# Optimization experiments

Measured on AMD Instinct MI355X. Metric: run time of the kernel, lower is better.

The kernel has to match this reference:

```python
import jax, jax.numpy as jnp
import numpy as np

B, T, IN, H, OUT = 128, 512, 64, 512, 1
H2 = H // 2


def setup_inputs() -> dict:
    key = jax.random.key(0)
    ks = jax.random.split(key, 16)
    s_in = 1.0 / np.sqrt(H)  # torch LSTM/Linear init scale ~ U(-1/sqrt(H), 1/sqrt(H))
    def u(k, shape, s):
        return jax.random.uniform(k, shape, jnp.float32, -s, s)
    return {
        "x": jax.random.normal(ks[0], (B, T, IN), jnp.float32),
        "W_ih0": u(ks[1], (4 * H, IN), s_in),
        "W_hh0": u(ks[2], (4 * H, H), s_in),
        "b_ih0": u(ks[3], (4 * H,), s_in),
        "b_hh0": u(ks[4], (4 * H,), s_in),
        "W_ih1": u(ks[5], (4 * H, H), s_in),
        "W_hh1": u(ks[6], (4 * H, H), s_in),
        "b_ih1": u(ks[7], (4 * H,), s_in),
        "b_hh1": u(ks[8], (4 * H,), s_in),
        "fc1_w": u(ks[9], (H2, H), s_in),
        "fc1_b": u(ks[10], (H2,), s_in),
        "fc2_w": u(ks[11], (OUT, H2), 1.0 / np.sqrt(H2)),
        "fc2_b": u(ks[12], (OUT,), 1.0 / np.sqrt(H2)),
    }


def _lstm_layer(x, W_ih, W_hh, b_ih, b_hh):
    # x: [B, T, D_in] -> outputs h for all timesteps [B, T, H]
    b, t, _ = x.shape
    h_dim = W_hh.shape[1]
    # precompute input contribution to gates for all timesteps: [T, B, 4H]
    xg = (jnp.einsum('btd,gd->btg', x, W_ih) + b_ih + b_hh).transpose(1, 0, 2)

    def step(carry, xt):
        h, c = carry
        gates = xt + h @ W_hh.T  # [B, 4H]
        i, f, g, o = jnp.split(gates, 4, axis=-1)  # torch gate order i,f,g,o
        i = jax.nn.sigmoid(i)
        f = jax.nn.sigmoid(f)
        g = jnp.tanh(g)
        o = jax.nn.sigmoid(o)
        c = f * c + i * g
        h = o * jnp.tanh(c)
        return (h, c), h

    h0 = jnp.zeros((b, h_dim), x.dtype)
    (_, _), hs = jax.lax.scan(step, (h0, h0), xg)
    return hs.transpose(1, 0, 2)  # [B, T, H]


def reference(x, W_ih0, W_hh0, b_ih0, b_hh0, W_ih1, W_hh1, b_ih1, b_hh1,
              fc1_w, fc1_b, fc2_w, fc2_b):
    h1 = _lstm_layer(x, W_ih0, W_hh0, b_ih0, b_hh0)
    h2 = _lstm_layer(h1, W_ih1, W_hh1, b_ih1, b_hh1)
    last = h2[:, -1, :]  # [B, H]
    z = jax.nn.relu(last @ fc1_w.T + fc1_b)
    return z @ fc2_w.T + fc2_b  # [B, OUT]
```

## Files before the change

kernel.cpp:

```cpp
#include <hip/hip_runtime.h>
#include <hip/hip_fp16.h>

#define BB   128
#define TT   512
#define INS  64
#define HH   512
#define K0   576
#define K1   1024
#define PAD0 584
#define PAD1 1032
#define H2   256
#define FS   16
#define RING 4

typedef _Float16 f16;
typedef f16 f16x4 __attribute__((ext_vector_type(4)));
typedef f16 f16x8 __attribute__((ext_vector_type(8)));
typedef float f32x4 __attribute__((ext_vector_type(4)));

__device__ __forceinline__ float sigmoidf_(float x) {
  return 1.0f / (1.0f + __expf(-x));
}
__device__ __forceinline__ float tanhf_(float x) {
  return 1.0f - 2.0f / (__expf(2.0f * x) + 1.0f);
}

__device__ __forceinline__ f16x8 ldg_h(const f16* p) {
  union { unsigned long long q[2]; f16x8 v; } u;
  const unsigned long long* qp = (const unsigned long long*)p;
  u.q[0] = __hip_atomic_load(qp,     __ATOMIC_RELAXED, __HIP_MEMORY_SCOPE_AGENT);
  u.q[1] = __hip_atomic_load(qp + 1, __ATOMIC_RELAXED, __HIP_MEMORY_SCOPE_AGENT);
  return u.v;
}
__device__ __forceinline__ void stg_h(f16* p, unsigned int pk) {
  __hip_atomic_store((unsigned int*)p, pk, __ATOMIC_RELAXED, __HIP_MEMORY_SCOPE_AGENT);
}
__device__ __forceinline__ int ldf(const int* p) {
  return __hip_atomic_load(p, __ATOMIC_RELAXED, __HIP_MEMORY_SCOPE_AGENT);
}

__global__ __launch_bounds__(256, 1) void lstm_persist(
    const float* __restrict__ x,
    const float* __restrict__ Wih0, const float* __restrict__ Whh0,
    const float* __restrict__ bih0, const float* __restrict__ bhh0,
    const float* __restrict__ Wih1, const float* __restrict__ Whh1,
    const float* __restrict__ bih1, const float* __restrict__ bhh1,
    int* __restrict__ flags, f16* __restrict__ h1ring, f16* __restrict__ h2ring)
{
  extern __shared__ f16 Ws[];

  const int tid  = threadIdx.x;
  const int wg   = blockIdx.x;
  const bool isL1 = (wg >= 128);
  const int w2   = wg & 127;
  const int mg   = w2 >> 6;
  const int ng   = w2 & 63;
  const int wid  = tid >> 6;
  const int lane = tid & 63;

  if (!isL1) {
    for (int e4 = tid; e4 < 32 * (K0 / 4); e4 += 256) {
      int r = e4 / (K0 / 4), k = (e4 - r * (K0 / 4)) * 4;
      int g = ((r >> 3) << 9) + (ng << 3) + (r & 7);
      float4 v = (k < INS)
          ? *reinterpret_cast<const float4*>(Wih0 + g * INS + k)
          : *reinterpret_cast<const float4*>(Whh0 + g * HH + (k - INS));
      f16x4 h; h[0]=(f16)v.x; h[1]=(f16)v.y; h[2]=(f16)v.z; h[3]=(f16)v.w;
      *reinterpret_cast<f16x4*>(&Ws[r * PAD0 + k]) = h;
    }
  } else {
    for (int e4 = tid; e4 < 32 * (K1 / 4); e4 += 256) {
      int r = e4 >> 8, k = (e4 & 255) * 4;
      int g = ((r >> 3) << 9) + (ng << 3) + (r & 7);
      float4 v = (k < HH)
          ? *reinterpret_cast<const float4*>(Wih1 + g * HH + k)
          : *reinterpret_cast<const float4*>(Whh1 + g * HH + (k - HH));
      f16x4 h; h[0]=(f16)v.x; h[1]=(f16)v.y; h[2]=(f16)v.z; h[3]=(f16)v.w;
      *reinterpret_cast<f16x4*>(&Ws[r * PAD1 + k]) = h;
    }
  }

  const int  wrow = mg * 64 + wid * 16;
  const int  row  = wrow + (lane & 15);
  const int  col0 = lane & 15;
  const int  kq   = (lane >> 4) * 8;
  const int  hcol = (ng << 3) + (lane & 7);
  const int  rowb = wrow + ((lane >> 4) << 2);
  const bool low  = (lane & 8) == 0;
  const bool evn  = (lane & 1) == 0;

  float bias[2];
  #pragma unroll
  for (int n = 0; n < 2; n++) {
    int c = n * 16 + col0;
    int g = ((c >> 3) << 9) + (ng << 3) + (c & 7);
    bias[n] = isL1 ? (bih1[g] + bhh1[g]) : (bih0[g] + bhh0[g]);
  }
  __syncthreads();

  int* f1 = flags + (mg)     * 256 * FS;
  int* f2 = flags + (2 + mg) * 256 * FS;
  int* myflag = (isL1 ? f2 : f1) + (ng * 4 + wid) * FS;

  f32x4 cst = {};

  if (!isL1) {
    for (int s = 0; s < TT; ++s) {
      const f16* h1r = h1ring + ((s + RING - 1) & (RING - 1)) * (BB * HH);
      f16*       h1w = h1ring + (s & (RING - 1)) * (BB * HH);

      const float* xb = x + ((size_t)row * TT + (size_t)s) * INS;
      float4 xq0 = *reinterpret_cast<const float4*>(xb + kq);
      float4 xq1 = *reinterpret_cast<const float4*>(xb + kq + 4);
      float4 xq2 = *reinterpret_cast<const float4*>(xb + 32 + kq);
      float4 xq3 = *reinterpret_cast<const float4*>(xb + 32 + kq + 4);

      int spin = 0;
      for (;;) {
        int m1 = ldf(f1 + (4 * lane + 0) * FS);
        m1 = min(m1, ldf(f1 + (4 * lane + 1) * FS));
        m1 = min(m1, ldf(f1 + (4 * lane + 2) * FS));
        m1 = min(m1, ldf(f1 + (4 * lane + 3) * FS));
        int m2 = ldf(f2 + (4 * lane + 0) * FS);
        m2 = min(m2, ldf(f2 + (4 * lane + 1) * FS));
        m2 = min(m2, ldf(f2 + (4 * lane + 2) * FS));
        m2 = min(m2, ldf(f2 + (4 * lane + 3) * FS));
        if (__all((m1 >= s) && (m2 >= s - 3))) break;
        if (++spin > (1 << 16)) break;
        __builtin_amdgcn_s_sleep(2);
      }
      asm volatile("" ::: "memory");

      f16x8 a[16];
      #pragma unroll
      for (int u = 0; u < 16; ++u)
        a[u] = ldg_h(h1r + row * HH + u * 32 + kq);

      f16x8 ax0, ax1;
      ax0[0]=(f16)xq0.x; ax0[1]=(f16)xq0.y; ax0[2]=(f16)xq0.z; ax0[3]=(f16)xq0.w;
      ax0[4]=(f16)xq1.x; ax0[5]=(f16)xq1.y; ax0[6]=(f16)xq1.z; ax0[7]=(f16)xq1.w;
      ax1[0]=(f16)xq2.x; ax1[1]=(f16)xq2.y; ax1[2]=(f16)xq2.z; ax1[3]=(f16)xq2.w;
      ax1[4]=(f16)xq3.x; ax1[5]=(f16)xq3.y; ax1[6]=(f16)xq3.z; ax1[7]=(f16)xq3.w;
      f32x4 acc0 = {}, acc1 = {};
      {
        f16x8 b;
        b = *reinterpret_cast<const f16x8*>(&Ws[col0 * PAD0 + kq]);
        acc0 = __builtin_amdgcn_mfma_f32_16x16x32_f16(ax0, b, acc0, 0, 0, 0);
        b = *reinterpret_cast<const f16x8*>(&Ws[(16 + col0) * PAD0 + kq]);
        acc1 = __builtin_amdgcn_mfma_f32_16x16x32_f16(ax0, b, acc1, 0, 0, 0);
        b = *reinterpret_cast<const f16x8*>(&Ws[col0 * PAD0 + 32 + kq]);
        acc0 = __builtin_amdgcn_mfma_f32_16x16x32_f16(ax1, b, acc0, 0, 0, 0);
        b = *reinterpret_cast<const f16x8*>(&Ws[(16 + col0) * PAD0 + 32 + kq]);
        acc1 = __builtin_amdgcn_mfma_f32_16x16x32_f16(ax1, b, acc1, 0, 0, 0);
      }
      #pragma unroll
      for (int u = 0; u < 16; ++u) {
        const int kk = INS + u * 32 + kq;
        f16x8 b0 = *reinterpret_cast<const f16x8*>(&Ws[col0 * PAD0 + kk]);
        f16x8 b1 = *reinterpret_cast<const f16x8*>(&Ws[(16 + col0) * PAD0 + kk]);
        acc0 = __builtin_amdgcn_mfma_f32_16x16x32_f16(a[u], b0, acc0, 0, 0, 0);
        acc1 = __builtin_amdgcn_mfma_f32_16x16x32_f16(a[u], b1, acc1, 0, 0, 0);
      }

      float res[4];
      #pragma unroll
      for (int j = 0; j < 4; j++) {
        float v0 = acc0[j] + bias[0];
        float v1 = acc1[j] + bias[1];
        float p0 = __shfl_xor(v0, 8, 64);
        float p1 = __shfl_xor(v1, 8, 64);
        float ip = low ? v0 : p0;
        float fp = low ? p0 : v0;
        float gp = low ? v1 : p1;
        float op = low ? p1 : v1;
        float cn = sigmoidf_(fp) * cst[j] + sigmoidf_(ip) * tanhf_(gp);
        cst[j] = cn;
        res[j] = sigmoidf_(op) * tanhf_(cn);
      }
      #pragma unroll
      for (int j = 0; j < 4; j++) {
        float other = __shfl_xor(res[j], 1, 64);
        if (low && evn) {
          f16 lo_ = (f16)res[j], hi_ = (f16)other;
          unsigned int pk =
              (unsigned int)__builtin_bit_cast(unsigned short, lo_) |
              ((unsigned int)__builtin_bit_cast(unsigned short, hi_) << 16);
          stg_h(h1w + (rowb + j) * HH + hcol, pk);
        }
      }
      asm volatile("s_waitcnt vmcnt(0)" ::: "memory");
      if (lane == 0)
        __hip_atomic_store(myflag, s + 1, __ATOMIC_RELAXED, __HIP_MEMORY_SCOPE_AGENT);
    }
  } else {
    for (int s = 1; s <= TT; ++s) {
      const f16* h1r = h1ring + ((s + RING - 1) & (RING - 1)) * (BB * HH);
      const f16* h2r = h2ring + ((s + RING - 2) & (RING - 1)) * (BB * HH);
      f16*       h2w = h2ring + ((s + RING - 1) & (RING - 1)) * (BB * HH);

      int spin = 0;
      for (;;) {
        int m1 = ldf(f1 + (4 * lane + 0) * FS);
        m1 = min(m1, ldf(f1 + (4 * lane + 1) * FS));
        m1 = min(m1, ldf(f1 + (4 * lane + 2) * FS));
        m1 = min(m1, ldf(f1 + (4 * lane + 3) * FS));
        int m2 = ldf(f2 + (4 * lane + 0) * FS);
        m2 = min(m2, ldf(f2 + (4 * lane + 1) * FS));
        m2 = min(m2, ldf(f2 + (4 * lane + 2) * FS));
        m2 = min(m2, ldf(f2 + (4 * lane + 3) * FS));
        if (__all((m1 >= s) && (m2 >= s - 1))) break;
        if (++spin > (1 << 16)) break;
        __builtin_amdgcn_s_sleep(2);
      }
      asm volatile("" ::: "memory");

      f16x8 a[32];
      #pragma unroll
      for (int u = 0; u < 16; ++u)
        a[u] = ldg_h(h1r + row * HH + u * 32 + kq);
      #pragma unroll
      for (int u = 0; u < 16; ++u)
        a[16 + u] = ldg_h(h2r + row * HH + u * 32 + kq);

      f32x4 acc0 = {}, acc1 = {};
      #pragma unroll
      for (int u = 0; u < 32; ++u) {
        const int kk = u * 32 + kq;
        f16x8 b0 = *reinterpret_cast<const f16x8*>(&Ws[col0 * PAD1 + kk]);
        f16x8 b1 = *reinterpret_cast<const f16x8*>(&Ws[(16 + col0) * PAD1 + kk]);
        acc0 = __builtin_amdgcn_mfma_f32_16x16x32_f16(a[u], b0, acc0, 0, 0, 0);
        acc1 = __builtin_amdgcn_mfma_f32_16x16x32_f16(a[u], b1, acc1, 0, 0, 0);
      }

      float res[4];
      #pragma unroll
      for (int j = 0; j < 4; j++) {
        float v0 = acc0[j] + bias[0];
        float v1 = acc1[j] + bias[1];
        float p0 = __shfl_xor(v0, 8, 64);
        float p1 = __shfl_xor(v1, 8, 64);
        float ip = low ? v0 : p0;
        float fp = low ? p0 : v0;
        float gp = low ? v1 : p1;
        float op = low ? p1 : v1;
        float cn = sigmoidf_(fp) * cst[j] + sigmoidf_(ip) * tanhf_(gp);
        cst[j] = cn;
        res[j] = sigmoidf_(op) * tanhf_(cn);
      }
      #pragma unroll
      for (int j = 0; j < 4; j++) {
        float other = __shfl_xor(res[j], 1, 64);
        if (low && evn) {
          f16 lo_ = (f16)res[j], hi_ = (f16)other;
          unsigned int pk =
              (unsigned int)__builtin_bit_cast(unsigned short, lo_) |
              ((unsigned int)__builtin_bit_cast(unsigned short, hi_) << 16);
          stg_h(h2w + (rowb + j) * HH + hcol, pk);
        }
      }
      asm volatile("s_waitcnt vmcnt(0)" ::: "memory");
      if (lane == 0)
        __hip_atomic_store(myflag, s, __ATOMIC_RELAXED, __HIP_MEMORY_SCOPE_AGENT);
    }
  }
}

__global__ void fc1_kernel(const f16* __restrict__ last, const float* __restrict__ w,
                           const float* __restrict__ b, float* __restrict__ z) {
  const int bb = blockIdx.x;
  const int j  = threadIdx.x;
  const f16*   lp = last + bb * HH;
  const float* wp = w + j * HH;
  float s = b[j];
  #pragma unroll 8
  for (int k = 0; k < HH; k++) s += (float)lp[k] * wp[k];
  z[bb * H2 + j] = fmaxf(s, 0.0f);
}

__global__ void fc2_kernel(const float* __restrict__ z, const float* __restrict__ w,
                           const float* __restrict__ b, float* __restrict__ out) {
  const int bb = threadIdx.x;
  float s = b[0];
  #pragma unroll 8
  for (int k = 0; k < H2; k++) s += z[bb * H2 + k] * w[k];
  out[bb] = s;
}

extern "C" void kernel_launch(void* const* d_in, const int* in_sizes, int n_in,
                              void* d_out, int out_size, void* d_ws, size_t ws_size,
                              hipStream_t stream) {
  const float* x     = (const float*)d_in[0];
  const float* Wih0  = (const float*)d_in[1];
  const float* Whh0  = (const float*)d_in[2];
  const float* bih0  = (const float*)d_in[3];
  const float* bhh0  = (const float*)d_in[4];
  const float* Wih1  = (const float*)d_in[5];
  const float* Whh1  = (const float*)d_in[6];
  const float* bih1  = (const float*)d_in[7];
  const float* bhh1  = (const float*)d_in[8];
  const float* fc1w  = (const float*)d_in[9];
  const float* fc1b  = (const float*)d_in[10];
  const float* fc2w  = (const float*)d_in[11];
  const float* fc2b  = (const float*)d_in[12];

  char* ws = (char*)d_ws;
  int*  flags = (int*)ws;
  const size_t FLAGS_B = (size_t)4 * 256 * FS * sizeof(int);
  f16*  h1 = (f16*)(ws + FLAGS_B);
  f16*  h2 = h1 + (size_t)RING * BB * HH;
  float* z = (float*)(ws + FLAGS_B + (size_t)2 * RING * BB * HH * sizeof(f16));

  hipMemsetAsync(ws, 0, FLAGS_B + (size_t)2 * RING * BB * HH * sizeof(f16), stream);

  const size_t smem = (size_t)32 * PAD1 * sizeof(f16);
  lstm_persist<<<256, 256, smem, stream>>>(x, Wih0, Whh0, bih0, bhh0,
                                           Wih1, Whh1, bih1, bhh1, flags, h1, h2);

  const f16* last = h2 + ((TT - 1) & (RING - 1)) * (BB * HH);
  fc1_kernel<<<BB, 256, 0, stream>>>(last, fc1w, fc1b, z);
  fc2_kernel<<<1, BB, 0, stream>>>(z, fc2w, fc2b, (float*)d_out);
}
```

Before: 8.392 ms.

## Replace per-wave flags with aggregated atomic arrival counters and split layer-1 loads

Each wave now signals with an atomic fetch_add on one of 16 shared counters per group, replacing its own flag slot. Consumers poll 32 cache lines instead of 512, and the s_sleep backoff becomes a short FMA busy-wait. Layer 1 also splits its A-operand loads so the h1 half is consumed by MFMAs before the h2 half is loaded, which halves register pressure. The costs are atomic contention on the shared counters (16 waves per counter) and heavier spinning on the memory system.

```diff
diff --git a/kernel.cpp b/kernel.cpp
--- a/kernel.cpp
+++ b/kernel.cpp
@@ -39,13 +39,34 @@
   return __hip_atomic_load(p, __ATOMIC_RELAXED, __HIP_MEMORY_SCOPE_AGENT);
 }
 
+__device__ __forceinline__ void poll_arrivals(const int* arr0, const int* arr1,
+                                              int t0, int t1, int lane) {
+  const int  myl = lane & 15;
+  const int* pp  = (lane < 16) ? (arr0 + myl * FS) : (arr1 + myl * FS);
+  const int  tgt = (lane < 16) ? t0 : t1;
+  const bool act = (lane < 32);
+  float bk = 1.0f;
+  int spin = 0;
+  for (;;) {
+    int v = act ? ldf(pp) : 0x7fffffff;
+    if (__all(v >= tgt)) break;
+    if (++spin > (1 << 18)) break;
+    float u = bk;
+    #pragma unroll
+    for (int i = 0; i < 16; i++) u = __builtin_fmaf(u, 1.000000119f, 1e-30f);
+    bk = u;
+    asm volatile("" : "+v"(bk));
+  }
+  asm volatile("" ::: "memory");
+}
+
 __global__ __launch_bounds__(256, 1) void lstm_persist(
     const float* __restrict__ x,
     const float* __restrict__ Wih0, const float* __restrict__ Whh0,
     const float* __restrict__ bih0, const float* __restrict__ bhh0,
     const float* __restrict__ Wih1, const float* __restrict__ Whh1,
     const float* __restrict__ bih1, const float* __restrict__ bhh1,
-    int* __restrict__ flags, f16* __restrict__ h1ring, f16* __restrict__ h2ring)
+    int* __restrict__ arr, f16* __restrict__ h1ring, f16* __restrict__ h2ring)
 {
   extern __shared__ f16 Ws[];
 
@@ -98,9 +119,9 @@
   }
   __syncthreads();
 
-  int* f1 = flags + (mg)     * 256 * FS;
-  int* f2 = flags + (2 + mg) * 256 * FS;
-  int* myflag = (isL1 ? f2 : f1) + (ng * 4 + wid) * FS;
+  int* arr0 = arr + (mg)     * 16 * FS;
+  int* arr1 = arr + (2 + mg) * 16 * FS;
+  int* myline = (isL1 ? arr1 : arr0) + (ng & 15) * FS;
 
   f32x4 cst = {};
 
@@ -115,21 +136,7 @@
       float4 xq2 = *reinterpret_cast<const float4*>(xb + 32 + kq);
       float4 xq3 = *reinterpret_cast<const float4*>(xb + 32 + kq + 4);
 
-      int spin = 0;
-      for (;;) {
-        int m1 = ldf(f1 + (4 * lane + 0) * FS);
-        m1 = min(m1, ldf(f1 + (4 * lane + 1) * FS));
-        m1 = min(m1, ldf(f1 + (4 * lane + 2) * FS));
-        m1 = min(m1, ldf(f1 + (4 * lane + 3) * FS));
-        int m2 = ldf(f2 + (4 * lane + 0) * FS);
-        m2 = min(m2, ldf(f2 + (4 * lane + 1) * FS));
-        m2 = min(m2, ldf(f2 + (4 * lane + 2) * FS));
-        m2 = min(m2, ldf(f2 + (4 * lane + 3) * FS));
-        if (__all((m1 >= s) && (m2 >= s - 3))) break;
-        if (++spin > (1 << 16)) break;
-        __builtin_amdgcn_s_sleep(2);
-      }
-      asm volatile("" ::: "memory");
+      poll_arrivals(arr0, arr1, 16 * s, 16 * (s - 3), lane);
 
       f16x8 a[16];
       #pragma unroll
@@ -190,7 +197,7 @@
       }
       asm volatile("s_waitcnt vmcnt(0)" ::: "memory");
       if (lane == 0)
-        __hip_atomic_store(myflag, s + 1, __ATOMIC_RELAXED, __HIP_MEMORY_SCOPE_AGENT);
+        __hip_atomic_fetch_add(myline, 1, __ATOMIC_RELAXED, __HIP_MEMORY_SCOPE_AGENT);
     }
   } else {
     for (int s = 1; s <= TT; ++s) {
@@ -198,34 +205,27 @@
       const f16* h2r = h2ring + ((s + RING - 2) & (RING - 1)) * (BB * HH);
       f16*       h2w = h2ring + ((s + RING - 1) & (RING - 1)) * (BB * HH);
 
-      int spin = 0;
-      for (;;) {
-        int m1 = ldf(f1 + (4 * lane + 0) * FS);
-        m1 = min(m1, ldf(f1 + (4 * lane + 1) * FS));
-        m1 = min(m1, ldf(f1 + (4 * lane + 2) * FS));
-        m1 = min(m1, ldf(f1 + (4 * lane + 3) * FS));
-        int m2 = ldf(f2 + (4 * lane + 0) * FS);
-        m2 = min(m2, ldf(f2 + (4 * lane + 1) * FS));
-        m2 = min(m2, ldf(f2 + (4 * lane + 2) * FS));
-        m2 = min(m2, ldf(f2 + (4 * lane + 3) * FS));
-        if (__all((m1 >= s) && (m2 >= s - 1))) break;
-        if (++spin > (1 << 16)) break;
-        __builtin_amdgcn_s_sleep(2);
-      }
-      asm volatile("" ::: "memory");
-
-      f16x8 a[32];
+      poll_arrivals(arr0, arr1, 16 * s, 16 * (s - 1), lane);
+
+      f16x8 a[16];
+      f32x4 acc0 = {}, acc1 = {};
       #pragma unroll
       for (int u = 0; u < 16; ++u)
         a[u] = ldg_h(h1r + row * HH + u * 32 + kq);
       #pragma unroll
+      for (int u = 0; u < 16; ++u) {
+        const int kk = u * 32 + kq;
+        f16x8 b0 = *reinterpret_cast<const f16x8*>(&Ws[col0 * PAD1 + kk]);
+        f16x8 b1 = *reinterpret_cast<const f16x8*>(&Ws[(16 + col0) * PAD1 + kk]);
+        acc0 = __builtin_amdgcn_mfma_f32_16x16x32_f16(a[u], b0, acc0, 0, 0, 0);
+        acc1 = __builtin_amdgcn_mfma_f32_16x16x32_f16(a[u], b1, acc1, 0, 0, 0);
+      }
+      #pragma unroll
       for (int u = 0; u < 16; ++u)
-        a[16 + u] = ldg_h(h2r + row * HH + u * 32 + kq);
-
-      f32x4 acc0 = {}, acc1 = {};
-      #pragma unroll
-      for (int u = 0; u < 32; ++u) {
-        const int kk = u * 32 + kq;
+        a[u] = ldg_h(h2r + row * HH + u * 32 + kq);
+      #pragma unroll
+      for (int u = 0; u < 16; ++u) {
+        const int kk = HH + u * 32 + kq;
         f16x8 b0 = *reinterpret_cast<const f16x8*>(&Ws[col0 * PAD1 + kk]);
         f16x8 b1 = *reinterpret_cast<const f16x8*>(&Ws[(16 + col0) * PAD1 + kk]);
         acc0 = __builtin_amdgcn_mfma_f32_16x16x32_f16(a[u], b0, acc0, 0, 0, 0);
@@ -260,7 +260,7 @@
       }
       asm volatile("s_waitcnt vmcnt(0)" ::: "memory");
       if (lane == 0)
-        __hip_atomic_store(myflag, s, __ATOMIC_RELAXED, __HIP_MEMORY_SCOPE_AGENT);
+        __hip_atomic_fetch_add(myline, 1, __ATOMIC_RELAXED, __HIP_MEMORY_SCOPE_AGENT);
     }
   }
 }
@@ -304,17 +304,17 @@
   const float* fc2b  = (const float*)d_in[12];
 
   char* ws = (char*)d_ws;
-  int*  flags = (int*)ws;
-  const size_t FLAGS_B = (size_t)4 * 256 * FS * sizeof(int);
-  f16*  h1 = (f16*)(ws + FLAGS_B);
+  int*  arr = (int*)ws;
+  const size_t ARR_B = (size_t)4 * 16 * FS * sizeof(int);
+  f16*  h1 = (f16*)(ws + ARR_B);
   f16*  h2 = h1 + (size_t)RING * BB * HH;
-  float* z = (float*)(ws + FLAGS_B + (size_t)2 * RING * BB * HH * sizeof(f16));
-
-  hipMemsetAsync(ws, 0, FLAGS_B + (size_t)2 * RING * BB * HH * sizeof(f16), stream);
+  float* z = (float*)(ws + ARR_B + (size_t)2 * RING * BB * HH * sizeof(f16));
+
+  hipMemsetAsync(ws, 0, ARR_B + (size_t)2 * RING * BB * HH * sizeof(f16), stream);
 
   const size_t smem = (size_t)32 * PAD1 * sizeof(f16);
   lstm_persist<<<256, 256, smem, stream>>>(x, Wih0, Whh0, bih0, bhh0,
-                                           Wih1, Whh1, bih1, bhh1, flags, h1, h2);
+                                           Wih1, Whh1, bih1, bhh1, arr, h1, h2);
 
   const f16* last = h2 + ((TT - 1) & (RING - 1)) * (BB * HH);
   fc1_kernel<<<BB, 256, 0, stream>>>(last, fc1w, fc1b, z);
```

After: 10.95 ms. 1.3x slower.

## Split LSTM batch into independent 16-row teams with register-resident weights

Applied to the files above, without the earlier changes.

Restructures the persistent LSTM kernel from 256 blocks that all synchronize across the full batch into 8 teams of 8 blocks, each team owning a 16-row batch slab and syncing only through its own 8 flags. Gate weights move from LDS into per-lane registers, and each step stages the team's hidden-state slab into double-buffered, XOR-swizzled LDS before the MFMA loop. A single wavefront polls the global flags and releases the rest of the block through an LDS variable, replacing sleep-based polling by every wave. The aim is to cut cross-CU synchronization latency and per-step traffic on the recurrent critical path. The cost is much heavier register pressure at 1024 threads per block, plus only 64 blocks in flight, so fewer CUs are used.

```diff
diff --git a/kernel.cpp b/kernel.cpp
--- a/kernel.cpp
+++ b/kernel.cpp
@@ -5,16 +5,17 @@
 #define TT   512
 #define INS  64
 #define HH   512
-#define K0   576
-#define K1   1024
-#define PAD0 584
-#define PAD1 1032
 #define H2   256
 #define FS   16
 #define RING 4
+#define SLAB 16
+#define BBHH (BB * HH)
+
+#define STR0 1040
+#define STR1 2064
+#define BUFB (16 * STR1)
 
 typedef _Float16 f16;
-typedef f16 f16x4 __attribute__((ext_vector_type(4)));
 typedef f16 f16x8 __attribute__((ext_vector_type(8)));
 typedef float f32x4 __attribute__((ext_vector_type(4)));
 
@@ -23,6 +24,12 @@
 }
 __device__ __forceinline__ float tanhf_(float x) {
   return 1.0f - 2.0f / (__expf(2.0f * x) + 1.0f);
+}
+__device__ __forceinline__ f16x8 pack8(float4 q0, float4 q1) {
+  f16x8 b;
+  b[0]=(f16)q0.x; b[1]=(f16)q0.y; b[2]=(f16)q0.z; b[3]=(f16)q0.w;
+  b[4]=(f16)q1.x; b[5]=(f16)q1.y; b[6]=(f16)q1.z; b[7]=(f16)q1.w;
+  return b;
 }
 
 __device__ __forceinline__ f16x8 ldg_h(const f16* p) {
@@ -39,7 +46,7 @@
   return __hip_atomic_load(p, __ATOMIC_RELAXED, __HIP_MEMORY_SCOPE_AGENT);
 }
 
-__global__ __launch_bounds__(256, 1) void lstm_persist(
+__global__ __launch_bounds__(1024, 1) void lstm_team(
     const float* __restrict__ x,
     const float* __restrict__ Wih0, const float* __restrict__ Whh0,
     const float* __restrict__ bih0, const float* __restrict__ bhh0,
@@ -47,119 +54,112 @@
     const float* __restrict__ bih1, const float* __restrict__ bhh1,
     int* __restrict__ flags, f16* __restrict__ h1ring, f16* __restrict__ h2ring)
 {
-  extern __shared__ f16 Ws[];
+  extern __shared__ char sm[];
+  __shared__ int s_ready;
 
   const int tid  = threadIdx.x;
-  const int wg   = blockIdx.x;
-  const bool isL1 = (wg >= 128);
-  const int w2   = wg & 127;
-  const int mg   = w2 >> 6;
-  const int ng   = w2 & 63;
+  const int team = blockIdx.x >> 3;
+  const int role = blockIdx.x & 7;
+  const bool isL1 = (role >= 4);
   const int wid  = tid >> 6;
   const int lane = tid & 63;
 
-  if (!isL1) {
-    for (int e4 = tid; e4 < 32 * (K0 / 4); e4 += 256) {
-      int r = e4 / (K0 / 4), k = (e4 - r * (K0 / 4)) * 4;
-      int g = ((r >> 3) << 9) + (ng << 3) + (r & 7);
-      float4 v = (k < INS)
-          ? *reinterpret_cast<const float4*>(Wih0 + g * INS + k)
-          : *reinterpret_cast<const float4*>(Whh0 + g * HH + (k - INS));
-      f16x4 h; h[0]=(f16)v.x; h[1]=(f16)v.y; h[2]=(f16)v.z; h[3]=(f16)v.w;
-      *reinterpret_cast<f16x4*>(&Ws[r * PAD0 + k]) = h;
-    }
-  } else {
-    for (int e4 = tid; e4 < 32 * (K1 / 4); e4 += 256) {
-      int r = e4 >> 8, k = (e4 & 255) * 4;
-      int g = ((r >> 3) << 9) + (ng << 3) + (r & 7);
-      float4 v = (k < HH)
-          ? *reinterpret_cast<const float4*>(Wih1 + g * HH + k)
-          : *reinterpret_cast<const float4*>(Whh1 + g * HH + (k - HH));
-      f16x4 h; h[0]=(f16)v.x; h[1]=(f16)v.y; h[2]=(f16)v.z; h[3]=(f16)v.w;
-      *reinterpret_cast<f16x4*>(&Ws[r * PAD1 + k]) = h;
-    }
-  }
-
-  const int  wrow = mg * 64 + wid * 16;
-  const int  row  = wrow + (lane & 15);
-  const int  col0 = lane & 15;
-  const int  kq   = (lane >> 4) * 8;
-  const int  hcol = (ng << 3) + (lane & 7);
-  const int  rowb = wrow + ((lane >> 4) << 2);
-  const bool low  = (lane & 8) == 0;
-  const bool evn  = (lane & 1) == 0;
+  const int ngx  = ((role & 3) << 4) + wid;
+  const int col0 = lane & 15;
+  const int kq2  = (lane >> 4) * 16;
+  const int rloc = lane & 15;
+  const int row  = team * SLAB + rloc;
+  const int hcol = (ngx << 3) + (lane & 7);
+  const int rowb = team * SLAB + ((lane >> 4) << 2);
+  const bool low = (lane & 8) == 0;
+  const bool evn = (lane & 1) == 0;
+  const int swz  = (rloc & 7) << 5;
+
+  const int sr = tid >> 6;
+  const int sc = tid & 63;
+  const int swzs = (sr & 7) << 5;
+
+  if (tid == 0) s_ready = -1;
 
   float bias[2];
   #pragma unroll
   for (int n = 0; n < 2; n++) {
-    int c = n * 16 + col0;
-    int g = ((c >> 3) << 9) + (ng << 3) + (c & 7);
+    const int c = n * 16 + col0;
+    const int g = ((c >> 3) << 9) + (ngx << 3) + (c & 7);
     bias[n] = isL1 ? (bih1[g] + bhh1[g]) : (bih0[g] + bhh0[g]);
   }
-  __syncthreads();
-
-  int* f1 = flags + (mg)     * 256 * FS;
-  int* f2 = flags + (2 + mg) * 256 * FS;
-  int* myflag = (isL1 ? f2 : f1) + (ng * 4 + wid) * FS;
+
+  int* tf     = flags + team * 8 * FS;
+  int* myflag = tf + role * FS;
 
   f32x4 cst = {};
 
   if (!isL1) {
+    f16x8 Bf[2][18];
+    #pragma unroll
+    for (int n = 0; n < 2; n++) {
+      const int c = n * 16 + col0;
+      const int g = ((c >> 3) << 9) + (ngx << 3) + (c & 7);
+      #pragma unroll
+      for (int ks = 0; ks < 18; ks++) {
+        const int k = ks * 32 + (kq2 >> 1);
+        const float* src = (k < INS) ? (Wih0 + (size_t)g * INS + k)
+                                     : (Whh0 + (size_t)g * HH + (k - INS));
+        Bf[n][ks] = pack8(*(const float4*)src, *(const float4*)(src + 4));
+      }
+    }
+    __syncthreads();
+
     for (int s = 0; s < TT; ++s) {
-      const f16* h1r = h1ring + ((s + RING - 1) & (RING - 1)) * (BB * HH);
-      f16*       h1w = h1ring + (s & (RING - 1)) * (BB * HH);
-
-      const float* xb = x + ((size_t)row * TT + (size_t)s) * INS;
-      float4 xq0 = *reinterpret_cast<const float4*>(xb + kq);
-      float4 xq1 = *reinterpret_cast<const float4*>(xb + kq + 4);
-      float4 xq2 = *reinterpret_cast<const float4*>(xb + 32 + kq);
-      float4 xq3 = *reinterpret_cast<const float4*>(xb + 32 + kq + 4);
-
-      int spin = 0;
-      for (;;) {
-        int m1 = ldf(f1 + (4 * lane + 0) * FS);
-        m1 = min(m1, ldf(f1 + (4 * lane + 1) * FS));
-        m1 = min(m1, ldf(f1 + (4 * lane + 2) * FS));
-        m1 = min(m1, ldf(f1 + (4 * lane + 3) * FS));
-        int m2 = ldf(f2 + (4 * lane + 0) * FS);
-        m2 = min(m2, ldf(f2 + (4 * lane + 1) * FS));
-        m2 = min(m2, ldf(f2 + (4 * lane + 2) * FS));
-        m2 = min(m2, ldf(f2 + (4 * lane + 3) * FS));
-        if (__all((m1 >= s) && (m2 >= s - 3))) break;
-        if (++spin > (1 << 16)) break;
-        __builtin_amdgcn_s_sleep(2);
-      }
-      asm volatile("" ::: "memory");
-
-      f16x8 a[16];
-      #pragma unroll
-      for (int u = 0; u < 16; ++u)
-        a[u] = ldg_h(h1r + row * HH + u * 32 + kq);
-
-      f16x8 ax0, ax1;
-      ax0[0]=(f16)xq0.x; ax0[1]=(f16)xq0.y; ax0[2]=(f16)xq0.z; ax0[3]=(f16)xq0.w;
-      ax0[4]=(f16)xq1.x; ax0[5]=(f16)xq1.y; ax0[6]=(f16)xq1.z; ax0[7]=(f16)xq1.w;
-      ax1[0]=(f16)xq2.x; ax1[1]=(f16)xq2.y; ax1[2]=(f16)xq2.z; ax1[3]=(f16)xq2.w;
-      ax1[4]=(f16)xq3.x; ax1[5]=(f16)xq3.y; ax1[6]=(f16)xq3.z; ax1[7]=(f16)xq3.w;
+      const f16* h1r = h1ring + ((s + 3) & 3) * BBHH;
+      f16*       h1w = h1ring + (s & 3) * BBHH;
+
+      if (wid == 0) {
+        const int tA = s, tB = s - 3;
+        int spin = 0; float bk = 1.0f;
+        for (;;) {
+          int v = (lane < 8) ? ldf(tf + lane * FS) : 0x7fffffff;
+          bool ok = (lane < 8) ? (v >= ((lane < 4) ? tA : tB)) : true;
+          if (__all(ok)) break;
+          if (++spin > (1 << 18)) break;
+          #pragma unroll
+          for (int i = 0; i < 32; i++) bk = __builtin_fmaf(bk, 1.0000001f, 1e-30f);
+          asm volatile("" : "+v"(bk));
+        }
+        asm volatile("" ::: "memory");
+        if (lane == 0)
+          __hip_atomic_store(&s_ready, s, __ATOMIC_RELEASE, __HIP_MEMORY_SCOPE_WORKGROUP);
+      }
+      {
+        int spin = 0; float bk = 1.0f;
+        while (__hip_atomic_load(&s_ready, __ATOMIC_ACQUIRE, __HIP_MEMORY_SCOPE_WORKGROUP) < s) {
+          if (++spin > (1 << 20)) break;
+          #pragma unroll
+          for (int i = 0; i < 8; i++) bk = __builtin_fmaf(bk, 1.0000001f, 1e-30f);
+          asm volatile("" : "+v"(bk));
+        }
+      }
+
+      char* buf = sm + (s & 1) * BUFB;
+      *(f16x8*)(buf + sr * STR0 + ((sc * 16) ^ swzs)) =
+          ldg_h(h1r + (size_t)(team * SLAB + sr) * HH + sc * 8);
+      __syncthreads();
+
+      const float* xb = x + ((size_t)row * TT + s) * INS;
+      const int kf = kq2 >> 1;
+      f16x8 ax0 = pack8(*(const float4*)(xb + kf), *(const float4*)(xb + kf + 4));
+      f16x8 ax1 = pack8(*(const float4*)(xb + 32 + kf), *(const float4*)(xb + 32 + kf + 4));
       f32x4 acc0 = {}, acc1 = {};
-      {
-        f16x8 b;
-        b = *reinterpret_cast<const f16x8*>(&Ws[col0 * PAD0 + kq]);
-        acc0 = __builtin_amdgcn_mfma_f32_16x16x32_f16(ax0, b, acc0, 0, 0, 0);
-        b = *reinterpret_cast<const f16x8*>(&Ws[(16 + col0) * PAD0 + kq]);
-        acc1 = __builtin_amdgcn_mfma_f32_16x16x32_f16(ax0, b, acc1, 0, 0, 0);
-        b = *reinterpret_cast<const f16x8*>(&Ws[col0 * PAD0 + 32 + kq]);
-        acc0 = __builtin_amdgcn_mfma_f32_16x16x32_f16(ax1, b, acc0, 0, 0, 0);
-        b = *reinterpret_cast<const f16x8*>(&Ws[(16 + col0) * PAD0 + 32 + kq]);
-        acc1 = __builtin_amdgcn_mfma_f32_16x16x32_f16(ax1, b, acc1, 0, 0, 0);
-      }
-      #pragma unroll
-      for (int u = 0; u < 16; ++u) {
-        const int kk = INS + u * 32 + kq;
-        f16x8 b0 = *reinterpret_cast<const f16x8*>(&Ws[col0 * PAD0 + kk]);
-        f16x8 b1 = *reinterpret_cast<const f16x8*>(&Ws[(16 + col0) * PAD0 + kk]);
-        acc0 = __builtin_amdgcn_mfma_f32_16x16x32_f16(a[u], b0, acc0, 0, 0, 0);
-        acc1 = __builtin_amdgcn_mfma_f32_16x16x32_f16(a[u], b1, acc1, 0, 0, 0);
+      acc0 = __builtin_amdgcn_mfma_f32_16x16x32_f16(ax0, Bf[0][0], acc0, 0, 0, 0);
+      acc1 = __builtin_amdgcn_mfma_f32_16x16x32_f16(ax0, Bf[1][0], acc1, 0, 0, 0);
+      acc0 = __builtin_amdgcn_mfma_f32_16x16x32_f16(ax1, Bf[0][1], acc0, 0, 0, 0);
+      acc1 = __builtin_amdgcn_mfma_f32_16x16x32_f16(ax1, Bf[1][1], acc1, 0, 0, 0);
+      const char* ab = buf + rloc * STR0;
+      #pragma unroll
+      for (int ks = 2; ks < 18; ks++) {
+        f16x8 a = *(const f16x8*)(ab + (((ks * 64 + kq2) - 128) ^ swz));
+        acc0 = __builtin_amdgcn_mfma_f32_16x16x32_f16(a, Bf[0][ks], acc0, 0, 0, 0);
+        acc1 = __builtin_amdgcn_mfma_f32_16x16x32_f16(a, Bf[1][ks], acc1, 0, 0, 0);
       }
 
       float res[4];
@@ -185,51 +185,78 @@
           unsigned int pk =
               (unsigned int)__builtin_bit_cast(unsigned short, lo_) |
               ((unsigned int)__builtin_bit_cast(unsigned short, hi_) << 16);
-          stg_h(h1w + (rowb + j) * HH + hcol, pk);
+          stg_h(h1w + (size_t)(rowb + j) * HH + hcol, pk);
         }
       }
       asm volatile("s_waitcnt vmcnt(0)" ::: "memory");
-      if (lane == 0)
+      __syncthreads();
+      if (tid == 0)
         __hip_atomic_store(myflag, s + 1, __ATOMIC_RELAXED, __HIP_MEMORY_SCOPE_AGENT);
     }
   } else {
-    for (int s = 1; s <= TT; ++s) {
-      const f16* h1r = h1ring + ((s + RING - 1) & (RING - 1)) * (BB * HH);
-      const f16* h2r = h2ring + ((s + RING - 2) & (RING - 1)) * (BB * HH);
-      f16*       h2w = h2ring + ((s + RING - 1) & (RING - 1)) * (BB * HH);
-
-      int spin = 0;
-      for (;;) {
-        int m1 = ldf(f1 + (4 * lane + 0) * FS);
-        m1 = min(m1, ldf(f1 + (4 * lane + 1) * FS));
-        m1 = min(m1, ldf(f1 + (4 * lane + 2) * FS));
-        m1 = min(m1, ldf(f1 + (4 * lane + 3) * FS));
-        int m2 = ldf(f2 + (4 * lane + 0) * FS);
-        m2 = min(m2, ldf(f2 + (4 * lane + 1) * FS));
-        m2 = min(m2, ldf(f2 + (4 * lane + 2) * FS));
-        m2 = min(m2, ldf(f2 + (4 * lane + 3) * FS));
-        if (__all((m1 >= s) && (m2 >= s - 1))) break;
-        if (++spin > (1 << 16)) break;
-        __builtin_amdgcn_s_sleep(2);
-      }
-      asm volatile("" ::: "memory");
-
-      f16x8 a[32];
-      #pragma unroll
-      for (int u = 0; u < 16; ++u)
-        a[u] = ldg_h(h1r + row * HH + u * 32 + kq);
-      #pragma unroll
-      for (int u = 0; u < 16; ++u)
-        a[16 + u] = ldg_h(h2r + row * HH + u * 32 + kq);
-
+    f16x8 Bf[2][32];
+    #pragma unroll
+    for (int n = 0; n < 2; n++) {
+      const int c = n * 16 + col0;
+      const int g = ((c >> 3) << 9) + (ngx << 3) + (c & 7);
+      #pragma unroll
+      for (int ks = 0; ks < 32; ks++) {
+        const int k = ks * 32 + (kq2 >> 1);
+        const float* src = (k < HH) ? (Wih1 + (size_t)g * HH + k)
+                                    : (Whh1 + (size_t)g * HH + (k - HH));
+        Bf[n][ks] = pack8(*(const float4*)src, *(const float4*)(src + 4));
+      }
+    }
+    __syncthreads();
+
+    for (int u = 0; u < TT; ++u) {
+      const f16* h1r = h1ring + (u & 3) * BBHH;
+      const f16* h2r = h2ring + ((u + 3) & 3) * BBHH;
+      f16*       h2w = h2ring + (u & 3) * BBHH;
+
+      if (wid == 0) {
+        const int tA = u + 1, tB = u;
+        int spin = 0; float bk = 1.0f;
+        for (;;) {
+          int v = (lane < 8) ? ldf(tf + lane * FS) : 0x7fffffff;
+          bool ok = (lane < 8) ? (v >= ((lane < 4) ? tA : tB)) : true;
+          if (__all(ok)) break;
+          if (++spin > (1 << 18)) break;
+          #pragma unroll
+          for (int i = 0; i < 32; i++) bk = __builtin_fmaf(bk, 1.0000001f, 1e-30f);
+          asm volatile("" : "+v"(bk));
+        }
+        asm volatile("" ::: "memory");
+        if (lane == 0)
+          __hip_atomic_store(&s_ready, u, __ATOMIC_RELEASE, __HIP_MEMORY_SCOPE_WORKGROUP);
+      }
+      {
+        int spin = 0; float bk = 1.0f;
+        while (__hip_atomic_load(&s_ready, __ATOMIC_ACQUIRE, __HIP_MEMORY_SCOPE_WORKGROUP) < u) {
+          if (++spin > (1 << 20)) break;
+          #pragma unroll
+          for (int i = 0; i < 8; i++) bk = __builtin_fmaf(bk, 1.0000001f, 1e-30f);
+          asm volatile("" : "+v"(bk));
+        }
+      }
+
+      char* buf = sm + (u & 1) * BUFB;
+      {
+        char* dst = buf + sr * STR1;
+        *(f16x8*)(dst + ((sc * 16) ^ swzs)) =
+            ldg_h(h1r + (size_t)(team * SLAB + sr) * HH + sc * 8);
+        *(f16x8*)(dst + 1024 + ((sc * 16) ^ swzs)) =
+            ldg_h(h2r + (size_t)(team * SLAB + sr) * HH + sc * 8);
+      }
+      __syncthreads();
+
+      const char* ab = buf + rloc * STR1;
       f32x4 acc0 = {}, acc1 = {};
       #pragma unroll
-      for (int u = 0; u < 32; ++u) {
-        const int kk = u * 32 + kq;
-        f16x8 b0 = *reinterpret_cast<const f16x8*>(&Ws[col0 * PAD1 + kk]);
-        f16x8 b1 = *reinterpret_cast<const f16x8*>(&Ws[(16 + col0) * PAD1 + kk]);
-        acc0 = __builtin_amdgcn_mfma_f32_16x16x32_f16(a[u], b0, acc0, 0, 0, 0);
-        acc1 = __builtin_amdgcn_mfma_f32_16x16x32_f16(a[u], b1, acc1, 0, 0, 0);
+      for (int ks = 0; ks < 32; ks++) {
+        f16x8 a = *(const f16x8*)(ab + ((ks * 64 + kq2) ^ swz));
+        acc0 = __builtin_amdgcn_mfma_f32_16x16x32_f16(a, Bf[0][ks], acc0, 0, 0, 0);
+        acc1 = __builtin_amdgcn_mfma_f32_16x16x32_f16(a, Bf[1][ks], acc1, 0, 0, 0);
       }
 
       float res[4];
@@ -255,12 +282,13 @@
           unsigned int pk =
               (unsigned int)__builtin_bit_cast(unsigned short, lo_) |
               ((unsigned int)__builtin_bit_cast(unsigned short, hi_) << 16);
-          stg_h(h2w + (rowb + j) * HH + hcol, pk);
+          stg_h(h2w + (size_t)(rowb + j) * HH + hcol, pk);
         }
       }
       asm volatile("s_waitcnt vmcnt(0)" ::: "memory");
-      if (lane == 0)
-        __hip_atomic_store(myflag, s, __ATOMIC_RELAXED, __HIP_MEMORY_SCOPE_AGENT);
+      __syncthreads();
+      if (tid == 0)
+        __hip_atomic_store(myflag, u + 1, __ATOMIC_RELAXED, __HIP_MEMORY_SCOPE_AGENT);
     }
   }
 }
@@ -305,18 +333,18 @@
 
   char* ws = (char*)d_ws;
   int*  flags = (int*)ws;
-  const size_t FLAGS_B = (size_t)4 * 256 * FS * sizeof(int);
+  const size_t FLAGS_B = 8192;
   f16*  h1 = (f16*)(ws + FLAGS_B);
-  f16*  h2 = h1 + (size_t)RING * BB * HH;
-  float* z = (float*)(ws + FLAGS_B + (size_t)2 * RING * BB * HH * sizeof(f16));
-
-  hipMemsetAsync(ws, 0, FLAGS_B + (size_t)2 * RING * BB * HH * sizeof(f16), stream);
-
-  const size_t smem = (size_t)32 * PAD1 * sizeof(f16);
-  lstm_persist<<<256, 256, smem, stream>>>(x, Wih0, Whh0, bih0, bhh0,
-                                           Wih1, Whh1, bih1, bhh1, flags, h1, h2);
-
-  const f16* last = h2 + ((TT - 1) & (RING - 1)) * (BB * HH);
+  f16*  h2 = h1 + (size_t)RING * BBHH;
+  float* z = (float*)(ws + FLAGS_B + (size_t)2 * RING * BBHH * sizeof(f16));
+
+  hipMemsetAsync(ws, 0, FLAGS_B + (size_t)2 * RING * BBHH * sizeof(f16), stream);
+
+  const size_t smem = 2 * BUFB;
+  lstm_team<<<64, 1024, smem, stream>>>(x, Wih0, Whh0, bih0, bhh0,
+                                        Wih1, Whh1, bih1, bhh1, flags, h1, h2);
+
+  const f16* last = h2 + ((TT - 1) & 3) * BBHH;
   fc1_kernel<<<BB, 256, 0, stream>>>(last, fc1w, fc1b, z);
   fc2_kernel<<<1, BB, 0, stream>>>(z, fc2w, fc2b, (float*)d_out);
 }
```

After: 14.28 ms. 1.7x slower.
